# Performance work log

Hardware: AMD Instinct MI355X
Metric: run time of the kernel (lower is better)

Reference implementation:

```python
import jax, jax.numpy as jnp
import numpy as np

B, H, W = 8, 1024, 1280
EPS = 1e-7
MIN_DEPTH, MAX_DEPTH = 10.0, 255.0


def _constants(batch, view_to_syn='left'):
    trans = np.array([-4.14339018, -0.0238197036, -0.00190685259], np.float32)
    K_u = np.array([1035.30811, 0.0, 596.955017, 0.0, 1035.08765, 520.410034, 0.0, 0.0, 1.0], np.float32).reshape(3, 3)
    K_u[0, :] /= 1280.0
    K_u[1, :] /= 1024.0
    K_u4 = np.zeros((4, 4), np.float32); K_u4[:3, :3] = K_u; K_u4[3, 3] = 1.0
    K_d = np.array([1035.17419, 0.0, 688.361877, 0.0, 1034.979, 521.070801, 0.0, 0.0, 1.0], np.float32).reshape(3, 3)
    K_d[0, :] /= 1280.0
    K_d[1, :] /= 1024.0
    K_d4 = np.zeros((4, 4), np.float32); K_d4[:3, :3] = K_d; K_d4[3, 3] = 1.0
    if view_to_syn == 'right':
        src, tgt, t = K_u4, K_d4, trans
    else:
        src, tgt, t = K_d4, K_u4, -trans
    source_K = jnp.asarray(np.tile(src[None], (batch, 1, 1)))
    target_K = jnp.asarray(np.tile(tgt[None], (batch, 1, 1)))
    trans_vec = jnp.asarray(np.tile(t[None], (batch, 1)))
    return source_K, target_K, trans_vec


def setup_inputs() -> dict:
    key = jax.random.key(0)
    k1, k2 = jax.random.split(key)
    img = jax.random.normal(k1, (B, 3, H, W), jnp.float32)
    pred_disp = jax.random.uniform(k2, (B, 1, H, W), jnp.float32)
    source_K, target_K, trans_vec = _constants(B, 'left')
    return {"img": img, "pred_disp": pred_disp, "source_K": source_K,
            "target_K": target_K, "trans_vec": trans_vec}


def _grid_sample_border(img, grid):
    """Bilinear grid_sample, padding_mode='border', align_corners=False (torch default).
    img: [B,C,H,W], grid: [B,H,W,2] in [-1,1] (x,y). Returns [B,C,H,W]."""
    b, c, h, w = img.shape
    x = (grid[..., 0] + 1.0) * w * 0.5 - 0.5  # [B,H,W]
    y = (grid[..., 1] + 1.0) * h * 0.5 - 0.5
    x0f = jnp.floor(x); y0f = jnp.floor(y)
    wx = (x - x0f)[:, None]  # [B,1,H,W]
    wy = (y - y0f)[:, None]
    x0 = jnp.clip(x0f.astype(jnp.int32), 0, w - 1)
    x1 = jnp.clip(x0f.astype(jnp.int32) + 1, 0, w - 1)
    y0 = jnp.clip(y0f.astype(jnp.int32), 0, h - 1)
    y1 = jnp.clip(y0f.astype(jnp.int32) + 1, 0, h - 1)
    gather = jax.vmap(lambda im, yi, xi: im[:, yi, xi])  # -> [B,C,H,W]
    i00 = gather(img, y0, x0)
    i01 = gather(img, y0, x1)
    i10 = gather(img, y1, x0)
    i11 = gather(img, y1, x1)
    return (i00 * (1 - wx) * (1 - wy) + i01 * wx * (1 - wy)
            + i10 * (1 - wx) * wy + i11 * wx * wy)


def reference(img, pred_disp, source_K, target_K, trans_vec):
    b, _, h, w = img.shape
    # disp -> depth
    min_disp, max_disp = 1.0 / MAX_DEPTH, 1.0 / MIN_DEPTH
    scaled_disp = min_disp + (max_disp - min_disp) * pred_disp
    depth = 1.0 / scaled_disp  # [B,1,H,W]
    # homogeneous pixel grid [3, H*W]
    xs, ys = jnp.meshgrid(jnp.arange(w, dtype=jnp.float32),
                          jnp.arange(h, dtype=jnp.float32), indexing='xy')
    pix = jnp.stack([xs.reshape(-1), ys.reshape(-1), jnp.ones(h * w, jnp.float32)], 0)
    # backproject
    inv_K = jnp.linalg.inv(source_K)[:, :3, :3]  # [B,3,3]
    cam = jnp.einsum('bij,jn->bin', inv_K, pix) * depth.reshape(b, 1, -1)  # [B,3,HW]
    cam4 = jnp.concatenate([cam, jnp.ones((b, 1, h * w), cam.dtype)], axis=1)  # [B,4,HW]
    # extrinsic: R = I, so T @ R = translation matrix
    T = jnp.tile(jnp.eye(4, dtype=img.dtype)[None], (b, 1, 1)).at[:, :3, 3].set(trans_vec.reshape(b, 3))
    P = jnp.matmul(target_K, T)[:, :3, :]  # [B,3,4]
    cp = jnp.matmul(P, cam4)  # [B,3,HW]
    pc = cp[:, :2] / (cp[:, 2:3] + EPS)  # [B,2,HW]
    pc = pc.reshape(b, 2, h, w).transpose(0, 2, 3, 1)  # [B,H,W,2]
    scale = jnp.array([w - 1, h - 1], dtype=pc.dtype)
    grid = (pc / scale - 0.5) * 2.0
    return _grid_sample_border(img, grid)
```

## Files before the change

### kernel.cpp

```cpp
#include <hip/hip_runtime.h>

#define BB 8
#define HH 1024
#define WW 1280
#define EPSF 1e-7f

__global__ __launch_bounds__(256) void synth_view_kernel(
    const float* __restrict__ img, const float* __restrict__ disp,
    const float* __restrict__ srcK, const float* __restrict__ tgtK,
    const float* __restrict__ trans, float* __restrict__ out)
{
    const int x = blockIdx.x * blockDim.x + threadIdx.x;
    const int y = blockIdx.y;
    const int b = blockIdx.z;
    if (x >= WW) return;

    const float* sK = srcK + b * 16;
    const float* tK = tgtK + b * 16;
    const float* tv = trans + b * 3;

    float a00 = sK[0], a01 = sK[1], a02 = sK[2];
    float a10 = sK[4], a11 = sK[5], a12 = sK[6];
    float a20 = sK[8], a21 = sK[9], a22 = sK[10];
    float det = a00*(a11*a22 - a12*a21)
              - a01*(a10*a22 - a12*a20)
              + a02*(a10*a21 - a11*a20);
    float rdet = 1.0f / det;
    float i00 =  (a11*a22 - a12*a21) * rdet;
    float i01 = -(a01*a22 - a02*a21) * rdet;
    float i02 =  (a01*a12 - a02*a11) * rdet;
    float i10 = -(a10*a22 - a12*a20) * rdet;
    float i11 =  (a00*a22 - a02*a20) * rdet;
    float i12 = -(a00*a12 - a02*a10) * rdet;
    float i20 =  (a10*a21 - a11*a20) * rdet;
    float i21 = -(a00*a21 - a01*a20) * rdet;
    float i22 =  (a00*a11 - a01*a10) * rdet;

    float t0 = tv[0], t1 = tv[1], t2 = tv[2];
    float p00 = tK[0],  p01 = tK[1],  p02 = tK[2];
    float p03 = tK[0]*t0 + tK[1]*t1 + tK[2]*t2 + tK[3];
    float p10 = tK[4],  p11 = tK[5],  p12 = tK[6];
    float p13 = tK[4]*t0 + tK[5]*t1 + tK[6]*t2 + tK[7];
    float p20 = tK[8],  p21 = tK[9],  p22 = tK[10];
    float p23 = tK[8]*t0 + tK[9]*t1 + tK[10]*t2 + tK[11];

    const long long pixidx = (long long)b * (HH * WW) + (long long)y * WW + x;
    float dsp = disp[pixidx];
    const float min_disp = 1.0f / 255.0f;
    const float max_disp = 1.0f / 10.0f;
    float depth = 1.0f / (min_disp + (max_disp - min_disp) * dsp);

    float fx = (float)x, fy = (float)y;
    float camx = (i00*fx + i01*fy + i02) * depth;
    float camy = (i10*fx + i11*fy + i12) * depth;
    float camz = (i20*fx + i21*fy + i22) * depth;

    float cpx = p00*camx + p01*camy + p02*camz + p03;
    float cpy = p10*camx + p11*camy + p12*camz + p13;
    float cpz = p20*camx + p21*camy + p22*camz + p23;

    float rz = 1.0f / (cpz + EPSF);
    float px = cpx * rz;
    float py = cpy * rz;

    float gx = (px / (float)(WW - 1) - 0.5f) * 2.0f;
    float gy = (py / (float)(HH - 1) - 0.5f) * 2.0f;
    float sx = (gx + 1.0f) * (float)WW * 0.5f - 0.5f;
    float sy = (gy + 1.0f) * (float)HH * 0.5f - 0.5f;

    float x0f = floorf(sx), y0f = floorf(sy);
    float wx = sx - x0f, wy = sy - y0f;
    int x0 = min(max((int)x0f,     0), WW - 1);
    int x1 = min(max((int)x0f + 1, 0), WW - 1);
    int y0 = min(max((int)y0f,     0), HH - 1);
    int y1 = min(max((int)y0f + 1, 0), HH - 1);

    float w00 = (1.0f - wx) * (1.0f - wy);
    float w01 = wx * (1.0f - wy);
    float w10 = (1.0f - wx) * wy;
    float w11 = wx * wy;

    const float* imb = img + (long long)b * 3 * HH * WW;
    long long o00 = (long long)y0 * WW + x0;
    long long o01 = (long long)y0 * WW + x1;
    long long o10 = (long long)y1 * WW + x0;
    long long o11 = (long long)y1 * WW + x1;
    float* outb = out + (long long)b * 3 * HH * WW + (long long)y * WW + x;

#pragma unroll
    for (int c = 0; c < 3; ++c) {
        const float* ic = imb + (long long)c * HH * WW;
        float v = ic[o00]*w00 + ic[o01]*w01 + ic[o10]*w10 + ic[o11]*w11;
        outb[(long long)c * HH * WW] = v;
    }
}

extern "C" void kernel_launch(void* const* d_in, const int* in_sizes, int n_in,
                              void* d_out, int out_size, void* d_ws, size_t ws_size,
                              hipStream_t stream) {
    const float* img   = (const float*)d_in[0];
    const float* disp  = (const float*)d_in[1];
    const float* srcK  = (const float*)d_in[2];
    const float* tgtK  = (const float*)d_in[3];
    const float* trans = (const float*)d_in[4];
    float* out = (float*)d_out;

    dim3 block(256, 1, 1);
    dim3 grid(WW / 256, HH, BB);
    synth_view_kernel<<<grid, block, 0, stream>>>(img, disp, srcK, tgtK, trans, out);
}
```

Baseline: 251.7 us.

## Simplify projection algebraically and process four pixels per thread with vector I/O

Collapses the inverse-intrinsics, projection and grid normalisation chain into a few per-batch affine coefficients, on the assumption that the K matrices are diagonal-plus-center with R = I. Each thread now handles four consecutive pixels, using a float4 nontemporal load for disparity and float4 nontemporal stores for the output. One 320-thread block covers a whole row. Fast reciprocals replace the IEEE divides, and 64-bit index math becomes 32-bit. The main risks are small numerical differences and reliance on zero skew and off-diagonal entries in K.

```diff
diff --git a/kernel.cpp b/kernel.cpp
--- a/kernel.cpp
+++ b/kernel.cpp
@@ -3,95 +3,103 @@
 #define BB 8
 #define HH 1024
 #define WW 1280
+#define HW (HH * WW)
 #define EPSF 1e-7f
 
-__global__ __launch_bounds__(256) void synth_view_kernel(
+typedef float f4 __attribute__((ext_vector_type(4)));
+
+__device__ __forceinline__ float fast_rcp(float x) {
+    float r = __builtin_amdgcn_rcpf(x);
+    r = r * __builtin_fmaf(-x, r, 2.0f);
+    return r;
+}
+
+__global__ __launch_bounds__(320) void synth_view_kernel(
     const float* __restrict__ img, const float* __restrict__ disp,
     const float* __restrict__ srcK, const float* __restrict__ tgtK,
     const float* __restrict__ trans, float* __restrict__ out)
 {
-    const int x = blockIdx.x * blockDim.x + threadIdx.x;
-    const int y = blockIdx.y;
-    const int b = blockIdx.z;
-    if (x >= WW) return;
+    const int tx = threadIdx.x;
+    const int xp = tx << 2;
+    const int y  = blockIdx.y;
+    const int b  = blockIdx.z;
 
     const float* sK = srcK + b * 16;
     const float* tK = tgtK + b * 16;
     const float* tv = trans + b * 3;
 
-    float a00 = sK[0], a01 = sK[1], a02 = sK[2];
-    float a10 = sK[4], a11 = sK[5], a12 = sK[6];
-    float a20 = sK[8], a21 = sK[9], a22 = sK[10];
-    float det = a00*(a11*a22 - a12*a21)
-              - a01*(a10*a22 - a12*a20)
-              + a02*(a10*a21 - a11*a20);
-    float rdet = 1.0f / det;
-    float i00 =  (a11*a22 - a12*a21) * rdet;
-    float i01 = -(a01*a22 - a02*a21) * rdet;
-    float i02 =  (a01*a12 - a02*a11) * rdet;
-    float i10 = -(a10*a22 - a12*a20) * rdet;
-    float i11 =  (a00*a22 - a02*a20) * rdet;
-    float i12 = -(a00*a12 - a02*a10) * rdet;
-    float i20 =  (a10*a21 - a11*a20) * rdet;
-    float i21 = -(a00*a21 - a01*a20) * rdet;
-    float i22 =  (a00*a11 - a01*a10) * rdet;
+    const float fsx = sK[0], csx = sK[2];
+    const float fsy = sK[5], csy = sK[6];
+    const float ftx = tK[0], ctx = tK[2];
+    const float fty = tK[5], cty = tK[6];
+    const float t0 = tv[0], t1 = tv[1], t2 = tv[2];
 
-    float t0 = tv[0], t1 = tv[1], t2 = tv[2];
-    float p00 = tK[0],  p01 = tK[1],  p02 = tK[2];
-    float p03 = tK[0]*t0 + tK[1]*t1 + tK[2]*t2 + tK[3];
-    float p10 = tK[4],  p11 = tK[5],  p12 = tK[6];
-    float p13 = tK[4]*t0 + tK[5]*t1 + tK[6]*t2 + tK[7];
-    float p20 = tK[8],  p21 = tK[9],  p22 = tK[10];
-    float p23 = tK[8]*t0 + tK[9]*t1 + tK[10]*t2 + tK[11];
+    const float Sx = (float)WW / (float)(WW - 1);
+    const float Sy = (float)HH / (float)(HH - 1);
+    const float rfsx = fast_rcp(fsx);
+    const float rfsy = fast_rcp(fsy);
+    const float A00 = ftx * rfsx * Sx;
+    const float A02 = __builtin_fmaf(-ftx * csx, rfsx, ctx) * Sx;
+    const float C0  = (ftx * t0 + ctx * t2) * Sx;
+    const float A11 = fty * rfsy * Sy;
+    const float A12 = __builtin_fmaf(-fty * csy, rfsy, cty) * Sy;
+    const float C1  = (fty * t1 + cty * t2) * Sy;
+    const float t2e = t2 + EPSF;
 
-    const long long pixidx = (long long)b * (HH * WW) + (long long)y * WW + x;
-    float dsp = disp[pixidx];
-    const float min_disp = 1.0f / 255.0f;
-    const float max_disp = 1.0f / 10.0f;
-    float depth = 1.0f / (min_disp + (max_disp - min_disp) * dsp);
+    const float ay = __builtin_fmaf(A11, (float)y, A12);
 
-    float fx = (float)x, fy = (float)y;
-    float camx = (i00*fx + i01*fy + i02) * depth;
-    float camy = (i10*fx + i11*fy + i12) * depth;
-    float camz = (i20*fx + i21*fy + i22) * depth;
+    const int rowoff = y * WW + xp;
+    const f4 d4 = __builtin_nontemporal_load(
+        reinterpret_cast<const f4*>(disp + b * HW + rowoff));
 
-    float cpx = p00*camx + p01*camy + p02*camz + p03;
-    float cpy = p10*camx + p11*camy + p12*camz + p13;
-    float cpz = p20*camx + p21*camy + p22*camz + p23;
+    const float mind = 1.0f / 255.0f;
+    const float rng  = 0.1f - mind;
 
-    float rz = 1.0f / (cpz + EPSF);
-    float px = cpx * rz;
-    float py = cpy * rz;
+    const float dk[4] = { d4.x, d4.y, d4.z, d4.w };
+    float w00[4], w01[4], w10[4], w11[4];
+    int   o00[4], o01[4], o10[4], o11[4];
 
-    float gx = (px / (float)(WW - 1) - 0.5f) * 2.0f;
-    float gy = (py / (float)(HH - 1) - 0.5f) * 2.0f;
-    float sx = (gx + 1.0f) * (float)WW * 0.5f - 0.5f;
-    float sy = (gy + 1.0f) * (float)HH * 0.5f - 0.5f;
+#pragma unroll
+    for (int k = 0; k < 4; ++k) {
+        const float sd = __builtin_fmaf(dk[k], rng, mind);
+        const float r  = fast_rcp(__builtin_fmaf(t2e, sd, 1.0f));
+        const float ax = __builtin_fmaf(A00, (float)(xp + k), A02);
+        const float sx = __builtin_fmaf(__builtin_fmaf(C0, sd, ax), r, -0.5f);
+        const float sy = __builtin_fmaf(__builtin_fmaf(C1, sd, ay), r, -0.5f);
 
-    float x0f = floorf(sx), y0f = floorf(sy);
-    float wx = sx - x0f, wy = sy - y0f;
-    int x0 = min(max((int)x0f,     0), WW - 1);
-    int x1 = min(max((int)x0f + 1, 0), WW - 1);
-    int y0 = min(max((int)y0f,     0), HH - 1);
-    int y1 = min(max((int)y0f + 1, 0), HH - 1);
+        const float xf = floorf(sx), yf = floorf(sy);
+        const float wx = sx - xf, wy = sy - yf;
+        const int ix = (int)xf, iy = (int)yf;
+        const int x0 = min(max(ix,     0), WW - 1);
+        const int x1 = min(max(ix + 1, 0), WW - 1);
+        const int y0 = min(max(iy,     0), HH - 1);
+        const int y1 = min(max(iy + 1, 0), HH - 1);
+        o00[k] = y0 * WW + x0;
+        o01[k] = y0 * WW + x1;
+        o10[k] = y1 * WW + x0;
+        o11[k] = y1 * WW + x1;
+        const float wxm = 1.0f - wx, wym = 1.0f - wy;
+        w00[k] = wxm * wym; w01[k] = wx * wym;
+        w10[k] = wxm * wy;  w11[k] = wx * wy;
+    }
 
-    float w00 = (1.0f - wx) * (1.0f - wy);
-    float w01 = wx * (1.0f - wy);
-    float w10 = (1.0f - wx) * wy;
-    float w11 = wx * wy;
-
-    const float* imb = img + (long long)b * 3 * HH * WW;
-    long long o00 = (long long)y0 * WW + x0;
-    long long o01 = (long long)y0 * WW + x1;
-    long long o10 = (long long)y1 * WW + x0;
-    long long o11 = (long long)y1 * WW + x1;
-    float* outb = out + (long long)b * 3 * HH * WW + (long long)y * WW + x;
+    const float* imb  = img + b * (3 * HW);
+    float*       outb = out + b * (3 * HW) + rowoff;
 
 #pragma unroll
     for (int c = 0; c < 3; ++c) {
-        const float* ic = imb + (long long)c * HH * WW;
-        float v = ic[o00]*w00 + ic[o01]*w01 + ic[o10]*w10 + ic[o11]*w11;
-        outb[(long long)c * HH * WW] = v;
+        const float* ic = imb + c * HW;
+        float v[4];
+#pragma unroll
+        for (int k = 0; k < 4; ++k) {
+            float acc =          ic[o00[k]] * w00[k];
+            acc = __builtin_fmaf(ic[o01[k]], w01[k], acc);
+            acc = __builtin_fmaf(ic[o10[k]], w10[k], acc);
+            acc = __builtin_fmaf(ic[o11[k]], w11[k], acc);
+            v[k] = acc;
+        }
+        f4 v4 = { v[0], v[1], v[2], v[3] };
+        __builtin_nontemporal_store(v4, reinterpret_cast<f4*>(outb + c * HW));
     }
 }
 
@@ -105,7 +113,7 @@
     const float* trans = (const float*)d_in[4];
     float* out = (float*)d_out;
 
-    dim3 block(256, 1, 1);
-    dim3 grid(WW / 256, HH, BB);
+    dim3 block(320, 1, 1);
+    dim3 grid(1, HH, BB);
     synth_view_kernel<<<grid, block, 0, stream>>>(img, disp, srcK, tgtK, trans, out);
 }
```

New measurement: 307.1 us. 22.0% more time.
